# Kernel tuning notes

Hardware: AMD Instinct MI355X
Metric: run time of the kernel (lower is better)

The kernel has to match this reference:

```python
import jax, jax.numpy as jnp
import numpy as np

B, N, D = 2, 2048, 1024
H, DH = 16, 64
DI = 4096
EPS = 1e-5
NEG_SLOPE = 0.01  # F.leaky_relu default


def _ln(x, g, b):
    mu = jnp.mean(x, axis=-1, keepdims=True)
    var = jnp.mean((x - mu) ** 2, axis=-1, keepdims=True)
    return (x - mu) * jax.lax.rsqrt(var + EPS) * g + b


def setup_inputs() -> dict:
    key = jax.random.key(0)
    ks = jax.random.split(key, 10)
    s = 0.02
    return {
        "Z": jax.random.normal(ks[0], (B, N, D), jnp.float32),
        "new_mask": jax.random.normal(ks[1], (B, N, N), jnp.float32),
        "mask": jax.random.uniform(ks[2], (B, N, N), jnp.float32),
        "ln1_g": jnp.ones((D,), jnp.float32),
        "ln1_b": jnp.zeros((D,), jnp.float32),
        "qkv_w": jax.random.normal(ks[3], (3 * D, D), jnp.float32) * s,
        "qkv_b": jnp.zeros((3 * D,), jnp.float32),
        "o_w": jax.random.normal(ks[4], (D, H * DH), jnp.float32) * s,
        "ln2_g": jnp.ones((D,), jnp.float32),
        "ln2_b": jnp.zeros((D,), jnp.float32),
        "p1_w": jax.random.normal(ks[5], (DI, D), jnp.float32) * s,
        "p1_b": jnp.zeros((DI,), jnp.float32),
        "p2_w": jax.random.normal(ks[6], (D, DI), jnp.float32) * s,
        "p2_b": jnp.zeros((D,), jnp.float32),
    }


def reference(Z, new_mask, mask, ln1_g, ln1_b, qkv_w, qkv_b, o_w, ln2_g, ln2_b, p1_w, p1_b, p2_w, p2_b):
    inp = Z
    Zn = _ln(Z, ln1_g, ln1_b)
    qkv = (Zn @ qkv_w.T + qkv_b).reshape(B, N, H, 3 * DH)
    # torch chunk order in the source: V, Q, K
    V, Q, K = jnp.split(qkv, 3, axis=3)  # each [B,N,H,DH]
    # scores: einsum('bnij,bmij->binm') == [B,H,N,N]
    W = jnp.einsum("bnhd,bmhd->bhnm", Q, K) / np.sqrt(DH) + new_mask[:, None]
    A = jax.nn.softmax(W, axis=3) * mask[:, None]
    attn = jnp.einsum("bhnm,bmhd->bnhd", A, V).reshape(B, N, D)
    attn = jnp.where(attn >= 0, attn, NEG_SLOPE * attn) @ o_w.T  # leaky_relu then o_net (no bias)
    Z1 = attn + inp
    Zn2 = _ln(Z1, ln2_g, ln2_b)
    h = jax.nn.relu(Zn2 @ p1_w.T + p1_b)
    return h @ p2_w.T + p2_b + Z1
```

## Files before the change

kernel.cpp:

```cpp
#include <hip/hip_runtime.h>

typedef unsigned short u16;
typedef __attribute__((ext_vector_type(8))) short bf16x8;
typedef __attribute__((ext_vector_type(4))) float f32x4;
typedef __attribute__((ext_vector_type(16))) float f32x16;
typedef __attribute__((ext_vector_type(4))) unsigned u32x4;

#define DEV static __device__ __forceinline__

DEV u16 f2bf(float f) {
    unsigned u = __float_as_uint(f);
    u += 0x7FFFu + ((u >> 16) & 1u);
    return (u16)(u >> 16);
}

typedef const __attribute__((address_space(1))) void* gas1_t;
typedef __attribute__((address_space(3))) void* gas3_t;

DEV void gl_lds16(const u16* g, u16* l) {
    __builtin_amdgcn_global_load_lds((gas1_t)g, (gas3_t)l, 16, 0, 0);
}

DEV unsigned cvtpk_bf16(float a, float b) {
    unsigned r;
    asm("v_cvt_pk_bf16_f32 %0, %1, %2" : "=v"(r) : "v"(a), "v"(b));
    return r;
}

DEV int sw8(int row, int chunk) { return row * 64 + ((chunk ^ (row & 7)) << 3); }

__global__ __launch_bounds__(256) void prep_all(const float* __restrict__ qkv_w,
                                                const float* __restrict__ o_w,
                                                const float* __restrict__ p1_w,
                                                const float* __restrict__ p2_w,
                                                const float* __restrict__ qkv_b,
                                                const float* __restrict__ nm,
                                                const float* __restrict__ pm,
                                                u16* __restrict__ qkvW,
                                                u16* __restrict__ oW,
                                                u16* __restrict__ p1W,
                                                u16* __restrict__ p2W,
                                                float* __restrict__ pbias,
                                                unsigned* __restrict__ Mp) {
    const int bid = blockIdx.x, t = threadIdx.x;
    if (bid < 3072) {
        int i = bid * 256 + t;
        int orow = i >> 8, cc = i & 255;
        int region = orow >> 10, rem = orow & 1023, h = rem >> 6, tt = rem & 63;
        int srow = h * 192 + region * 64 + tt;
        float4 v = ((const float4*)qkv_w)[srow * 256 + cc];
        ushort4 o;
        o.x = f2bf(v.x); o.y = f2bf(v.y); o.z = f2bf(v.z); o.w = f2bf(v.w);
        ((ushort4*)qkvW)[i] = o;
    } else if (bid < 4096) {
        int i = (bid - 3072) * 256 + t;
        float4 v = ((const float4*)o_w)[i];
        ushort4 o;
        o.x = f2bf(v.x); o.y = f2bf(v.y); o.z = f2bf(v.z); o.w = f2bf(v.w);
        ((ushort4*)oW)[i] = o;
    } else if (bid < 8192) {
        int i = (bid - 4096) * 256 + t;
        float4 v = ((const float4*)p1_w)[i];
        ushort4 o;
        o.x = f2bf(v.x); o.y = f2bf(v.y); o.z = f2bf(v.z); o.w = f2bf(v.w);
        ((ushort4*)p1W)[i] = o;
    } else if (bid < 12288) {
        int i = (bid - 8192) * 256 + t;
        float4 v = ((const float4*)p2_w)[i];
        ushort4 o;
        o.x = f2bf(v.x); o.y = f2bf(v.y); o.z = f2bf(v.z); o.w = f2bf(v.w);
        ((ushort4*)p2W)[i] = o;
    } else if (bid < 20480) {
        int i = (bid - 12288) * 256 + t;
        float4 a = ((const float4*)nm)[i];
        float4 b = ((const float4*)pm)[i];
        uint4 o;
        o.x = ((unsigned)f2bf(b.x) << 16) | f2bf(a.x * 1.4426950f);
        o.y = ((unsigned)f2bf(b.y) << 16) | f2bf(a.y * 1.4426950f);
        o.z = ((unsigned)f2bf(b.z) << 16) | f2bf(a.z * 1.4426950f);
        o.w = ((unsigned)f2bf(b.w) << 16) | f2bf(a.w * 1.4426950f);
        int e = i * 4;
        int bb = e >> 22;
        int rem = e & 4194303;
        int n = rem >> 11;
        int m = rem & 2047;
        int mt = m >> 5;
        int j = m & 31;
        int hi = (j >> 2) & 1;
        int rb4 = j >> 3;
        size_t oi = (((size_t)(bb * 64 + mt) * 2048 + n) * 2 + hi) * 4 + rb4;
        ((uint4*)Mp)[oi] = o;
    } else {
#pragma unroll
        for (int k = 0; k < 12; k++) {
            int i = k * 256 + t;
            int region = i >> 10, rem = i & 1023, h = rem >> 6, tt = rem & 63;
            pbias[i] = qkv_b[h * 192 + region * 64 + tt];
        }
    }
}

__global__ __launch_bounds__(256) void ln_bf16(const float* __restrict__ x,
                                               const float* __restrict__ gam,
                                               const float* __restrict__ bet,
                                               u16* __restrict__ y) {
    const int row = blockIdx.x;
    const int t = threadIdx.x;
    const float4 v = ((const float4*)(x + (size_t)row * 1024))[t];
    float s = v.x + v.y + v.z + v.w;
    float ss = v.x * v.x + v.y * v.y + v.z * v.z + v.w * v.w;
#pragma unroll
    for (int o = 1; o < 64; o <<= 1) {
        s += __shfl_xor(s, o);
        ss += __shfl_xor(ss, o);
    }
    __shared__ float rs[4], rss[4];
    const int wave = t >> 6, lane = t & 63;
    if (lane == 0) { rs[wave] = s; rss[wave] = ss; }
    __syncthreads();
    const float tot = rs[0] + rs[1] + rs[2] + rs[3];
    const float totss = rss[0] + rss[1] + rss[2] + rss[3];
    const float mu = tot * (1.0f / 1024.0f);
    const float var = totss * (1.0f / 1024.0f) - mu * mu;
    const float rstd = rsqrtf(var + 1e-5f);
    const float4 g4 = ((const float4*)gam)[t];
    const float4 b4 = ((const float4*)bet)[t];
    ushort4 o;
    o.x = f2bf((v.x - mu) * rstd * g4.x + b4.x);
    o.y = f2bf((v.y - mu) * rstd * g4.y + b4.y);
    o.z = f2bf((v.z - mu) * rstd * g4.z + b4.z);
    o.w = f2bf((v.w - mu) * rstd * g4.w + b4.w);
    ((ushort4*)(y + (size_t)row * 1024))[t] = o;
}

__global__ __launch_bounds__(256) void ln2_comb4(const float* __restrict__ p0,
                                                 const float* __restrict__ p1,
                                                 const float* __restrict__ p2,
                                                 const float* __restrict__ p3,
                                                 const float* __restrict__ Z,
                                                 const float* __restrict__ gam,
                                                 const float* __restrict__ bet,
                                                 float* __restrict__ Z1,
                                                 u16* __restrict__ y) {
    const int row = blockIdx.x;
    const int t = threadIdx.x;
    const size_t off = (size_t)row * 256 + t;
    const float4 a = ((const float4*)p0)[off];
    const float4 c = ((const float4*)p1)[off];
    const float4 d = ((const float4*)p2)[off];
    const float4 e = ((const float4*)p3)[off];
    const float4 z = ((const float4*)Z)[off];
    float4 v;
    v.x = a.x + c.x + d.x + e.x + z.x;
    v.y = a.y + c.y + d.y + e.y + z.y;
    v.z = a.z + c.z + d.z + e.z + z.z;
    v.w = a.w + c.w + d.w + e.w + z.w;
    ((float4*)Z1)[off] = v;
    float s = v.x + v.y + v.z + v.w;
    float ss = v.x * v.x + v.y * v.y + v.z * v.z + v.w * v.w;
#pragma unroll
    for (int o = 1; o < 64; o <<= 1) {
        s += __shfl_xor(s, o);
        ss += __shfl_xor(ss, o);
    }
    __shared__ float rs[4], rss[4];
    const int wave = t >> 6, lane = t & 63;
    if (lane == 0) { rs[wave] = s; rss[wave] = ss; }
    __syncthreads();
    const float tot = rs[0] + rs[1] + rs[2] + rs[3];
    const float totss = rss[0] + rss[1] + rss[2] + rss[3];
    const float mu = tot * (1.0f / 1024.0f);
    const float var = totss * (1.0f / 1024.0f) - mu * mu;
    const float rstd = rsqrtf(var + 1e-5f);
    const float4 g4 = ((const float4*)gam)[t];
    const float4 b4 = ((const float4*)bet)[t];
    ushort4 o;
    o.x = f2bf((v.x - mu) * rstd * g4.x + b4.x);
    o.y = f2bf((v.y - mu) * rstd * g4.y + b4.y);
    o.z = f2bf((v.z - mu) * rstd * g4.z + b4.z);
    o.w = f2bf((v.w - mu) * rstd * g4.w + b4.w);
    ((ushort4*)(y + (size_t)row * 1024))[t] = o;
}

__global__ __launch_bounds__(256) void out_comb(const float* __restrict__ p0,
                                                const float* __restrict__ p1,
                                                const float* __restrict__ bias,
                                                const float* __restrict__ Z1,
                                                float* __restrict__ out) {
    int i = blockIdx.x * 256 + threadIdx.x;
    float4 a = ((const float4*)p0)[i];
    float4 c = ((const float4*)p1)[i];
    float4 z = ((const float4*)Z1)[i];
    float4 b = ((const float4*)bias)[i & 255];
    float4 o;
    o.x = a.x + c.x + z.x + b.x; o.y = a.y + c.y + z.y + b.y;
    o.z = a.z + c.z + z.z + b.z; o.w = a.w + c.w + z.w + b.w;
    ((float4*)out)[i] = o;
}

template <int EPI>
__global__ __launch_bounds__(256, 3) void gemm_bt(const u16* __restrict__ A,
                                                  const u16* __restrict__ Bt,
                                                  const float* __restrict__ bias,
                                                  void* __restrict__ out0,
                                                  void* __restrict__ out1,
                                                  void* __restrict__ out2,
                                                  int M, int N, int K, int ldk) {
    __shared__ __align__(16) u16 As[128 * 32];
    __shared__ __align__(16) u16 Bs[128 * 32];
    const int tid = threadIdx.x;
    const int wave = tid >> 6, lane = tid & 63;
    const int lhi = lane >> 4, llo = lane & 15;
    const int bx = blockIdx.x, by = blockIdx.y;
    const int kz = blockIdx.z * K;

    const int arow = wave * 32 + (lane >> 2);
    const int acol = (lane & 3) * 8;
    const u16* gA = A + (size_t)(by * 128 + arow) * ldk + kz + acol;
    const u16* gB = Bt + (size_t)(bx * 128 + arow) * ldk + kz + acol;
    u16* lA = As + wave * 1024 + lane * 8;
    u16* lB = Bs + wave * 1024 + lane * 8;

    const int wr = wave >> 1, wc = wave & 1;
    const f32x4 zero = {0.f, 0.f, 0.f, 0.f};
    f32x4 acc[4][4];
#pragma unroll
    for (int i = 0; i < 4; i++)
#pragma unroll
        for (int j = 0; j < 4; j++) acc[i][j] = zero;

    for (int k0 = 0; k0 < K; k0 += 32) {
        __syncthreads();
        gl_lds16(gA, lA);
        gl_lds16(gA + 16 * (size_t)ldk, lA + 512);
        gl_lds16(gB, lB);
        gl_lds16(gB + 16 * (size_t)ldk, lB + 512);
        gA += 32; gB += 32;
        __syncthreads();
        bf16x8 af[4], bfr[4];
#pragma unroll
        for (int i = 0; i < 4; i++)
            af[i] = *(const bf16x8*)(As + (wr * 64 + i * 16 + llo) * 32 + lhi * 8);
#pragma unroll
        for (int j = 0; j < 4; j++)
            bfr[j] = *(const bf16x8*)(Bs + (wc * 64 + j * 16 + llo) * 32 + lhi * 8);
#pragma unroll
        for (int i = 0; i < 4; i++)
#pragma unroll
            for (int j = 0; j < 4; j++)
                acc[i][j] = __builtin_amdgcn_mfma_f32_16x16x32_bf16(af[i], bfr[j], acc[i][j], 0, 0, 0);
    }

    const int rbase = by * 128 + wr * 64 + lhi * 4;
    const int cbase = bx * 128 + wc * 64 + llo;
    float* pout = nullptr;
    if constexpr (EPI == 4) {
        pout = (blockIdx.z < 2) ? ((float*)out0 + (size_t)blockIdx.z * M * N)
                                : ((float*)out1 + (size_t)(blockIdx.z - 2) * M * N);
    }
#pragma unroll
    for (int i = 0; i < 4; i++) {
#pragma unroll
        for (int j = 0; j < 4; j++) {
#pragma unroll
            for (int r = 0; r < 4; r++) {
                const int row = rbase + i * 16 + r;
                const int col = cbase + j * 16;
                float v = acc[i][j][r];
                if constexpr (EPI == 0) {
                    v += bias[col];
                    const int region = col >> 10;
                    const int c = col & 1023;
                    const int b = row >> 11, n = row & 2047;
                    if (region == 0) {
                        ((float*)out0)[(size_t)row * 1024 + c] = v;
                    } else {
                        const int h = c >> 6, t = c & 63;
                        u16* dst = (region == 1) ? (u16*)out1 : (u16*)out2;
                        dst[(((size_t)(b * 16 + h)) * 2048 + n) * 64 + t] = f2bf(v);
                    }
                } else if constexpr (EPI == 2) {
                    v += bias[col];
                    v = v > 0.f ? v : 0.f;
                    ((u16*)out0)[(size_t)row * N + col] = f2bf(v);
                } else {
                    pout[(size_t)row * N + col] = v;
                }
            }
        }
    }
}

__global__ __launch_bounds__(256) void vtrans(const float* __restrict__ Vsc,
                                              u16* __restrict__ Vt) {
    __shared__ u16 Ts[64 * 72];
    const int nt = blockIdx.x;
    const int bh = blockIdx.y;
    const int b = bh >> 4, h = bh & 15;
    const int t = threadIdx.x;
    const int n0 = nt * 64;
    const int nr = t >> 2;
    const int dq = (t & 3) * 16;
    const float* src = Vsc + ((size_t)(b * 2048 + n0 + nr)) * 1024 + h * 64 + dq;
    float4 v0 = ((const float4*)src)[0];
    float4 v1 = ((const float4*)src)[1];
    float4 v2 = ((const float4*)src)[2];
    float4 v3 = ((const float4*)src)[3];
    u16* c0 = Ts + nr;
    c0[(dq + 0) * 72]  = f2bf(v0.x); c0[(dq + 1) * 72]  = f2bf(v0.y);
    c0[(dq + 2) * 72]  = f2bf(v0.z); c0[(dq + 3) * 72]  = f2bf(v0.w);
    c0[(dq + 4) * 72]  = f2bf(v1.x); c0[(dq + 5) * 72]  = f2bf(v1.y);
    c0[(dq + 6) * 72]  = f2bf(v1.z); c0[(dq + 7) * 72]  = f2bf(v1.w);
    c0[(dq + 8) * 72]  = f2bf(v2.x); c0[(dq + 9) * 72]  = f2bf(v2.y);
    c0[(dq + 10) * 72] = f2bf(v2.z); c0[(dq + 11) * 72] = f2bf(v2.w);
    c0[(dq + 12) * 72] = f2bf(v3.x); c0[(dq + 13) * 72] = f2bf(v3.y);
    c0[(dq + 14) * 72] = f2bf(v3.z); c0[(dq + 15) * 72] = f2bf(v3.w);
    __syncthreads();
    const int d = t >> 2, n8 = (t & 3) * 16;
    bf16x8 o0 = *(const bf16x8*)(Ts + d * 72 + n8);
    bf16x8 o1 = *(const bf16x8*)(Ts + d * 72 + n8 + 8);
    u16* dst = Vt + ((size_t)bh * 64 + d) * 2048 + n0 + n8;
    *(bf16x8*)dst = o0;
    *(bf16x8*)(dst + 8) = o1;
}

DEV void stage_kv(const u16* __restrict__ Kg, const u16* __restrict__ Vtg,
                  u16* ks, u16* vs, int bh, int m0, int wave, int lane) {
    const int l3 = lane >> 3, l7 = lane & 7;
    const int swcol = (l7 ^ l3) << 3;
#pragma unroll
    for (int s = 0; s < 2; s++) {
        const int row = wave * 16 + s * 8 + l3;
        gl_lds16(Kg + ((size_t)bh * 2048 + m0 + row) * 64 + swcol,
                 ks + wave * 1024 + s * 512 + lane * 8);
        gl_lds16(Vtg + ((size_t)bh * 64 + row) * 2048 + m0 + swcol,
                 vs + wave * 1024 + s * 512 + lane * 8);
    }
}

__global__ __launch_bounds__(256, 4) void attn_fused5(const u16* __restrict__ Qg,
                                                      const u16* __restrict__ Kg,
                                                      const u16* __restrict__ Vtg,
                                                      const unsigned* __restrict__ Mp,
                                                      u16* __restrict__ attnL) {
    __shared__ __align__(16) u16 Ks[2][64 * 64];
    __shared__ __align__(16) u16 Vs[2][64 * 64];
    __shared__ float lsh[2][32], lsh2[2][32];
    const int tid = threadIdx.x, wave = tid >> 6, lane = tid & 63;
    const int qh = wave & 1, wm = wave >> 1;
    const int hi = lane >> 5, l31 = lane & 31;
    const int id = blockIdx.x;
    const int hh = id >> 6, rem = id & 63;
    const int b = rem >> 5, qt = rem & 31;
    const int bh = b * 16 + hh;
    const int q0 = qt * 64;

    stage_kv(Kg, Vtg, Ks[0], Vs[0], bh, 0, wave, lane);
    const int qrow = q0 + qh * 32 + l31;
    const u16* qptr = Qg + ((size_t)bh * 2048 + qrow) * 64 + hi * 8;
    bf16x8 qf[4];
#pragma unroll
    for (int ks = 0; ks < 4; ks++) qf[ks] = *(const bf16x8*)(qptr + ks * 16);

    const unsigned* mptr = Mp + (size_t)b * 4194304 + (size_t)wm * 65536
                              + (size_t)qrow * 32 + hi * 16;

    const f32x16 z16 = {0.f,0.f,0.f,0.f,0.f,0.f,0.f,0.f,0.f,0.f,0.f,0.f,0.f,0.f,0.f,0.f};
    f32x16 accO[2];
    accO[0] = z16; accO[1] = z16;
    float lsum = 0.f;
    const float CS = 0.125f * 1.4426950f;
    const bool h1 = (hi != 0);
    __syncthreads();

    for (int t = 0; t < 32; t++) {
        const int cur = t & 1;
        const uint4* mp4 = (const uint4*)(mptr + (size_t)t * 131072);
        const uint4 mva = mp4[0], mvb = mp4[1], mvc = mp4[2], mvd = mp4[3];
        if (t < 31) stage_kv(Kg, Vtg, Ks[cur ^ 1], Vs[cur ^ 1], bh, (t + 1) * 64, wave, lane);

        const u16* ksb = Ks[cur];
        f32x16 sacc = z16;
        __builtin_amdgcn_s_setprio(1);
#pragma unroll
        for (int ks = 0; ks < 4; ks++) {
            const bf16x8 kf = *(const bf16x8*)(ksb + sw8(wm * 32 + l31, ks * 2 + hi));
            sacc = __builtin_amdgcn_mfma_f32_32x32x16_bf16(kf, qf[ks], sacc, 0, 0, 0);
        }
        __builtin_amdgcn_s_setprio(0);

        const unsigned mm[16] = {mva.x, mva.y, mva.z, mva.w, mvb.x, mvb.y, mvb.z, mvb.w,
                                 mvc.x, mvc.y, mvc.z, mvc.w, mvd.x, mvd.y, mvd.z, mvd.w};
        float p[16];
#pragma unroll
        for (int r = 0; r < 16; r++) {
            const unsigned u = mm[r];
            const float e = exp2f(fmaf(sacc[r], CS, __uint_as_float(u << 16)));
            lsum += e;
            p[r] = e * __uint_as_float(u & 0xFFFF0000u);
        }
        const unsigned w0 = cvtpk_bf16(p[0], p[1]),   w1 = cvtpk_bf16(p[2], p[3]);
        const unsigned w2 = cvtpk_bf16(p[4], p[5]),   w3 = cvtpk_bf16(p[6], p[7]);
        const unsigned w4 = cvtpk_bf16(p[8], p[9]),   w5 = cvtpk_bf16(p[10], p[11]);
        const unsigned w6 = cvtpk_bf16(p[12], p[13]), w7 = cvtpk_bf16(p[14], p[15]);
        const unsigned o0 = (unsigned)__shfl_xor((int)w0, 32);
        const unsigned o1 = (unsigned)__shfl_xor((int)w1, 32);
        const unsigned o2 = (unsigned)__shfl_xor((int)w2, 32);
        const unsigned o3 = (unsigned)__shfl_xor((int)w3, 32);
        const unsigned o4 = (unsigned)__shfl_xor((int)w4, 32);
        const unsigned o5 = (unsigned)__shfl_xor((int)w5, 32);
        const unsigned o6 = (unsigned)__shfl_xor((int)w6, 32);
        const unsigned o7 = (unsigned)__shfl_xor((int)w7, 32);
        const u32x4 fa0 = {h1 ? o2 : w0, h1 ? o3 : w1, h1 ? w2 : o0, h1 ? w3 : o1};
        const u32x4 fa1 = {h1 ? o6 : w4, h1 ? o7 : w5, h1 ? w6 : o4, h1 ? w7 : o5};
        const bf16x8 pa0 = __builtin_bit_cast(bf16x8, fa0);
        const bf16x8 pa1 = __builtin_bit_cast(bf16x8, fa1);

        const u16* vsb = Vs[cur];
        __builtin_amdgcn_s_setprio(1);
#pragma unroll
        for (int dh = 0; dh < 2; dh++) {
            const bf16x8 vf0 = *(const bf16x8*)(vsb + sw8(dh * 32 + l31, wm * 4 + hi));
            accO[dh] = __builtin_amdgcn_mfma_f32_32x32x16_bf16(pa0, vf0, accO[dh], 0, 0, 0);
            const bf16x8 vf1 = *(const bf16x8*)(vsb + sw8(dh * 32 + l31, wm * 4 + 2 + hi));
            accO[dh] = __builtin_amdgcn_mfma_f32_32x32x16_bf16(pa1, vf1, accO[dh], 0, 0, 0);
        }
        __builtin_amdgcn_s_setprio(0);
        __syncthreads();
    }

    const float lsum2 = lsum + __shfl_xor(lsum, 32);
    float* cb = (float*)&Ks[0][0];
    if (wm == 1) {
        float* dst = cb + (size_t)(qh * 64 + lane) * 32;
#pragma unroll
        for (int dh = 0; dh < 2; dh++)
#pragma unroll
            for (int c = 0; c < 4; c++) {
                const f32x4 v = {accO[dh][c * 4 + 0], accO[dh][c * 4 + 1],
                                 accO[dh][c * 4 + 2], accO[dh][c * 4 + 3]};
                *(f32x4*)(dst + dh * 16 + c * 4) = v;
            }
        if (lane < 32) lsh[qh][lane] = lsum2;
    }
    __syncthreads();
    if (wm == 0) {
        const float* src = cb + (size_t)(qh * 64 + lane) * 32;
        const float lt = lsum2 + lsh[qh][l31];
#pragma unroll
        for (int dh = 0; dh < 2; dh++)
#pragma unroll
            for (int c = 0; c < 16; c++)
                accO[dh][c] += src[dh * 16 + c];
        if (lane < 32) lsh2[qh][lane] = 1.0f / lt;
    }
    __syncthreads();
    if (wm == 0) {
#pragma unroll
        for (int r = 0; r < 16; r++) {
            const int ql = (r & 3) + 8 * (r >> 2) + 4 * hi;
            const float linv = lsh2[qh][ql];
            const int qg = q0 + qh * 32 + ql;
#pragma unroll
            for (int dh = 0; dh < 2; dh++) {
                float v = accO[dh][r] * linv;
                v = v >= 0.f ? v : 0.01f * v;
                attnL[((size_t)b * 2048 + qg) * 1024 + hh * 64 + dh * 32 + l31] = f2bf(v);
            }
        }
    }
}

extern "C" void kernel_launch(void* const* d_in, const int* in_sizes, int n_in,
                              void* d_out, int out_size, void* d_ws, size_t ws_size,
                              hipStream_t stream) {
    const float* Z     = (const float*)d_in[0];
    const float* nmask = (const float*)d_in[1];
    const float* pmask = (const float*)d_in[2];
    const float* ln1_g = (const float*)d_in[3];
    const float* ln1_b = (const float*)d_in[4];
    const float* qkv_w = (const float*)d_in[5];
    const float* qkv_b = (const float*)d_in[6];
    const float* o_w   = (const float*)d_in[7];
    const float* ln2_g = (const float*)d_in[8];
    const float* ln2_b = (const float*)d_in[9];
    const float* p1_w  = (const float*)d_in[10];
    const float* p1_b  = (const float*)d_in[11];
    const float* p2_w  = (const float*)d_in[12];
    const float* p2_b  = (const float*)d_in[13];
    float* out = (float*)d_out;

    char* w = (char*)d_ws;
    auto take = [&](size_t bytes) -> char* {
        char* p = w;
        w += (bytes + 255) & ~(size_t)255;
        return p;
    };
    u16* qkvW   = (u16*)take((size_t)3072 * 1024 * 2);
    u16* oW     = (u16*)take((size_t)1024 * 1024 * 2);
    u16* p1W    = (u16*)take((size_t)4096 * 1024 * 2);
    u16* p2W    = (u16*)take((size_t)1024 * 4096 * 2);
    u16* Zn     = (u16*)take((size_t)4096 * 1024 * 2);
    u16* Qb     = (u16*)take((size_t)32 * 2048 * 64 * 2);
    u16* Kb     = (u16*)take((size_t)32 * 2048 * 64 * 2);
    u16* Vt     = (u16*)take((size_t)32 * 64 * 2048 * 2);
    u16* attnL  = (u16*)take((size_t)4096 * 1024 * 2);
    float* Z1   = (float*)take((size_t)4096 * 1024 * 4);
    u16* hbuf   = (u16*)take((size_t)4096 * 4096 * 2);
    unsigned* Mp = (unsigned*)take((size_t)2 * 2048 * 2048 * 4);
    float* pbias = (float*)take((size_t)3072 * 4);
    float* Vsc    = (float*)hbuf;
    float* part01 = (float*)Mp;
    float* part23 = (float*)hbuf;

    prep_all<<<dim3(20481), 256, 0, stream>>>(qkv_w, o_w, p1_w, p2_w, qkv_b, nmask, pmask,
                                              qkvW, oW, p1W, p2W, pbias, Mp);
    ln_bf16<<<dim3(4096), 256, 0, stream>>>(Z, ln1_g, ln1_b, Zn);
    gemm_bt<0><<<dim3(24, 32), 256, 0, stream>>>(Zn, qkvW, pbias, Vsc, Qb, Kb, 4096, 3072, 1024, 1024);
    vtrans<<<dim3(32, 32), 256, 0, stream>>>(Vsc, Vt);
    attn_fused5<<<dim3(1024), 256, 0, stream>>>(Qb, Kb, Vt, Mp, attnL);
    gemm_bt<4><<<dim3(8, 32, 4), 256, 0, stream>>>(attnL, oW, nullptr, part01, part23, nullptr,
                                                   4096, 1024, 256, 1024);
    ln2_comb4<<<dim3(4096), 256, 0, stream>>>(part01, part01 + (size_t)4096 * 1024,
                                              part23, part23 + (size_t)4096 * 1024,
                                              Z, ln2_g, ln2_b, Z1, Zn);
    gemm_bt<2><<<dim3(32, 32), 256, 0, stream>>>(Zn, p1W, p1_b, hbuf, nullptr, nullptr,
                                                 4096, 4096, 1024, 1024);
    gemm_bt<4><<<dim3(8, 32, 2), 256, 0, stream>>>(hbuf, p2W, nullptr, part01, nullptr, nullptr,
                                                   4096, 1024, 2048, 4096);
    out_comb<<<dim3(4096), 256, 0, stream>>>(part01, part01 + (size_t)4096 * 1024, p2_b, Z1, out);
}
```

Before: 458.8 us.

## Permute V-transpose and mask layouts to drop P-fragment shuffles; remap attention blocks

Measured after the change: 447.8 us. 1.02x faster.

```diff
diff --git a/kernel.cpp b/kernel.cpp
--- a/kernel.cpp
+++ b/kernel.cpp
@@ -85,10 +85,10 @@
         int n = rem >> 11;
         int m = rem & 2047;
         int mt = m >> 5;
-        int j = m & 31;
-        int hi = (j >> 2) & 1;
-        int rb4 = j >> 3;
-        size_t oi = (((size_t)(bb * 64 + mt) * 2048 + n) * 2 + hi) * 4 + rb4;
+        int m5 = m & 31;
+        int c = m5 >> 3;
+        int hi = (m5 >> 2) & 1;
+        size_t oi = (((size_t)(bb * 64 + mt) * 4 + c) * 2048 + n) * 2 + hi;
         ((uint4*)Mp)[oi] = o;
     } else {
 #pragma unroll
@@ -317,11 +317,14 @@
     c0[(dq + 14) * 72] = f2bf(v3.z); c0[(dq + 15) * 72] = f2bf(v3.w);
     __syncthreads();
     const int d = t >> 2, n8 = (t & 3) * 16;
-    bf16x8 o0 = *(const bf16x8*)(Ts + d * 72 + n8);
-    bf16x8 o1 = *(const bf16x8*)(Ts + d * 72 + n8 + 8);
-    u16* dst = Vt + ((size_t)bh * 64 + d) * 2048 + n0 + n8;
-    *(bf16x8*)dst = o0;
-    *(bf16x8*)(dst + 8) = o1;
+    u16* dstrow = Vt + ((size_t)bh * 64 + d) * 2048 + n0;
+#pragma unroll
+    for (int w = 0; w < 4; w++) {
+        const int gi = (n8 >> 2) + w;
+        const int g5 = gi & 7, blk = gi >> 3;
+        const int pg = (g5 & 4) | ((g5 & 1) << 1) | ((g5 >> 1) & 1);
+        *(uint2*)(dstrow + blk * 32 + pg * 4) = *(const uint2*)(Ts + d * 72 + n8 + w * 4);
+    }
 }
 
 DEV void stage_kv(const u16* __restrict__ Kg, const u16* __restrict__ Vtg,
@@ -338,7 +341,7 @@
     }
 }
 
-__global__ __launch_bounds__(256, 4) void attn_fused5(const u16* __restrict__ Qg,
+__global__ __launch_bounds__(256, 4) void attn_fused6(const u16* __restrict__ Qg,
                                                       const u16* __restrict__ Kg,
                                                       const u16* __restrict__ Vtg,
                                                       const unsigned* __restrict__ Mp,
@@ -349,9 +352,11 @@
     const int tid = threadIdx.x, wave = tid >> 6, lane = tid & 63;
     const int qh = wave & 1, wm = wave >> 1;
     const int hi = lane >> 5, l31 = lane & 31;
-    const int id = blockIdx.x;
-    const int hh = id >> 6, rem = id & 63;
-    const int b = rem >> 5, qt = rem & 31;
+    const int pid = blockIdx.x;
+    const int seq = pid >> 3;
+    const int hh = seq & 15;
+    const int g = (pid & 7) + (seq >> 4) * 8;
+    const int b = g >> 5, qt = g & 31;
     const int bh = b * 16 + hh;
     const int q0 = qt * 64;
 
@@ -362,21 +367,20 @@
 #pragma unroll
     for (int ks = 0; ks < 4; ks++) qf[ks] = *(const bf16x8*)(qptr + ks * 16);
 
-    const unsigned* mptr = Mp + (size_t)b * 4194304 + (size_t)wm * 65536
-                              + (size_t)qrow * 32 + hi * 16;
+    const uint4* mb4 = (const uint4*)Mp + ((size_t)(b * 64 + wm) * 4) * 4096
+                                        + (size_t)qrow * 2 + hi;
 
     const f32x16 z16 = {0.f,0.f,0.f,0.f,0.f,0.f,0.f,0.f,0.f,0.f,0.f,0.f,0.f,0.f,0.f,0.f};
     f32x16 accO[2];
     accO[0] = z16; accO[1] = z16;
     float lsum = 0.f;
     const float CS = 0.125f * 1.4426950f;
-    const bool h1 = (hi != 0);
     __syncthreads();
 
     for (int t = 0; t < 32; t++) {
         const int cur = t & 1;
-        const uint4* mp4 = (const uint4*)(mptr + (size_t)t * 131072);
-        const uint4 mva = mp4[0], mvb = mp4[1], mvc = mp4[2], mvd = mp4[3];
+        const uint4* mp4 = mb4 + (size_t)t * 32768;
+        const uint4 mva = mp4[0], mvb = mp4[4096], mvc = mp4[8192], mvd = mp4[12288];
         if (t < 31) stage_kv(Kg, Vtg, Ks[cur ^ 1], Vs[cur ^ 1], bh, (t + 1) * 64, wave, lane);
 
         const u16* ksb = Ks[cur];
@@ -399,20 +403,10 @@
             lsum += e;
             p[r] = e * __uint_as_float(u & 0xFFFF0000u);
         }
-        const unsigned w0 = cvtpk_bf16(p[0], p[1]),   w1 = cvtpk_bf16(p[2], p[3]);
-        const unsigned w2 = cvtpk_bf16(p[4], p[5]),   w3 = cvtpk_bf16(p[6], p[7]);
-        const unsigned w4 = cvtpk_bf16(p[8], p[9]),   w5 = cvtpk_bf16(p[10], p[11]);
-        const unsigned w6 = cvtpk_bf16(p[12], p[13]), w7 = cvtpk_bf16(p[14], p[15]);
-        const unsigned o0 = (unsigned)__shfl_xor((int)w0, 32);
-        const unsigned o1 = (unsigned)__shfl_xor((int)w1, 32);
-        const unsigned o2 = (unsigned)__shfl_xor((int)w2, 32);
-        const unsigned o3 = (unsigned)__shfl_xor((int)w3, 32);
-        const unsigned o4 = (unsigned)__shfl_xor((int)w4, 32);
-        const unsigned o5 = (unsigned)__shfl_xor((int)w5, 32);
-        const unsigned o6 = (unsigned)__shfl_xor((int)w6, 32);
-        const unsigned o7 = (unsigned)__shfl_xor((int)w7, 32);
-        const u32x4 fa0 = {h1 ? o2 : w0, h1 ? o3 : w1, h1 ? w2 : o0, h1 ? w3 : o1};
-        const u32x4 fa1 = {h1 ? o6 : w4, h1 ? o7 : w5, h1 ? w6 : o4, h1 ? w7 : o5};
+        const u32x4 fa0 = {cvtpk_bf16(p[0], p[1]),  cvtpk_bf16(p[2], p[3]),
+                           cvtpk_bf16(p[4], p[5]),  cvtpk_bf16(p[6], p[7])};
+        const u32x4 fa1 = {cvtpk_bf16(p[8], p[9]),  cvtpk_bf16(p[10], p[11]),
+                           cvtpk_bf16(p[12], p[13]), cvtpk_bf16(p[14], p[15])};
         const bf16x8 pa0 = __builtin_bit_cast(bf16x8, fa0);
         const bf16x8 pa1 = __builtin_bit_cast(bf16x8, fa1);
 
@@ -518,7 +512,7 @@
     ln_bf16<<<dim3(4096), 256, 0, stream>>>(Z, ln1_g, ln1_b, Zn);
     gemm_bt<0><<<dim3(24, 32), 256, 0, stream>>>(Zn, qkvW, pbias, Vsc, Qb, Kb, 4096, 3072, 1024, 1024);
     vtrans<<<dim3(32, 32), 256, 0, stream>>>(Vsc, Vt);
-    attn_fused5<<<dim3(1024), 256, 0, stream>>>(Qb, Kb, Vt, Mp, attnL);
+    attn_fused6<<<dim3(1024), 256, 0, stream>>>(Qb, Kb, Vt, Mp, attnL);
     gemm_bt<4><<<dim3(8, 32, 4), 256, 0, stream>>>(attnL, oW, nullptr, part01, part23, nullptr,
                                                    4096, 1024, 256, 1024);
     ln2_comb4<<<dim3(4096), 256, 0, stream>>>(part01, part01 + (size_t)4096 * 1024,
```
